# Performance work log

Measured on AMD Instinct MI355X. Metric: run time of the kernel, lower is better.

## Reference

```python
import jax, jax.numpy as jnp
import numpy as np

WIN = 7
K1, K2 = 0.01, 0.03
NP_ = WIN ** 3
COV_NORM = NP_ / (NP_ - 1)


def _box3d(x, win=WIN):
    # Separable box filter: three 1D VALID convs (same math as the dense
    for ax in range(3):
        kshape = [1, 1, 1, 1, 1]
        kshape[2 + ax] = win
        k = jnp.ones(kshape, x.dtype) / win
        x = jax.lax.conv_general_dilated(
            x, k, window_strides=(1, 1, 1), padding='VALID',
            dimension_numbers=('NCDHW', 'OIDHW', 'NCDHW'))
    return x


def setup_inputs() -> dict:
    key = jax.random.key(0)
    k1, k2 = jax.random.split(key)
    B, C, D, H, W = 4, 1, 128, 128, 128
    X = jax.random.normal(k1, (B, C, D, H, W), dtype=jnp.float32)
    Y = jax.random.normal(k2, (B, C, D, H, W), dtype=jnp.float32)
    data_range = jnp.ones((B, 1, 1, 1, 1), dtype=jnp.float32)
    return {"X": X, "Y": Y, "data_range": data_range}


def reference(X, Y, data_range):
    C1 = (K1 * data_range) ** 2
    C2 = (K2 * data_range) ** 2
    ux = _box3d(X)
    uy = _box3d(Y)
    uxx = _box3d(X * X)
    uyy = _box3d(Y * Y)
    uxy = _box3d(X * Y)
    vx = COV_NORM * (uxx - ux * ux)
    vy = COV_NORM * (uyy - uy * uy)
    vxy = COV_NORM * (uxy - ux * uy)
    A1 = 2 * ux * uy + C1
    A2 = 2 * vxy + C2
    B1 = ux ** 2 + uy ** 2 + C1
    B2 = vx + vy + C2
    S = (A1 * A2) / (B1 * B2)
    return S.mean()
```

## Files before the change

kernel.cpp:

```cpp
#include <hip/hip_runtime.h>

#define NFULL 128
#define NOUT  122

#define S1_R 34
#define S1_Q 748
#define S2_R 34
#define S2_Q 546
#define NBLK 1024

__device__ __forceinline__ void phaseA_task(const float* __restrict__ px,
                                            const float* __restrict__ py,
                                            float* __restrict__ s1p)
{
    float xs[8], ys[8];
#pragma unroll
    for (int k = 0; k < 4; ++k) {
        float2 tx = *(const float2*)(px + 2 * k);
        float2 ty = *(const float2*)(py + 2 * k);
        xs[2 * k] = tx.x; xs[2 * k + 1] = tx.y;
        ys[2 * k] = ty.x; ys[2 * k + 1] = ty.y;
    }
    float sx = 0.f, sy = 0.f, sxx = 0.f, syy = 0.f, sxy = 0.f;
#pragma unroll
    for (int k = 0; k < 7; ++k) {
        sx += xs[k]; sy += ys[k];
        sxx = fmaf(xs[k], xs[k], sxx);
        syy = fmaf(ys[k], ys[k], syy);
        sxy = fmaf(xs[k], ys[k], sxy);
    }
    float tx2 = sx - xs[0] + xs[7];
    float ty2 = sy - ys[0] + ys[7];
    float txx = sxx - xs[0] * xs[0] + xs[7] * xs[7];
    float tyy = syy - ys[0] * ys[0] + ys[7] * ys[7];
    float txy = sxy - xs[0] * ys[0] + xs[7] * ys[7];
    *(float2*)(s1p + 0 * S1_Q) = make_float2(sx,  tx2);
    *(float2*)(s1p + 1 * S1_Q) = make_float2(sy,  ty2);
    *(float2*)(s1p + 2 * S1_Q) = make_float2(sxx, txx);
    *(float2*)(s1p + 3 * S1_Q) = make_float2(syy, tyy);
    *(float2*)(s1p + 4 * S1_Q) = make_float2(sxy, txy);
}

__global__ __launch_bounds__(256, 4)
void ssim3d_kernel(const float* __restrict__ X, const float* __restrict__ Y,
                   const float* __restrict__ DR, double* __restrict__ ws, int mode)
{
    __shared__ __align__(16) float s1[5 * S1_Q];
    __shared__ __align__(16) float s2[5 * S2_Q];

    const int tid = threadIdx.x;
    int bi = blockIdx.x;
    const int bb = bi & 3;  bi >>= 2;
    const int ht = bi & 7;  bi >>= 3;
    const int wt = bi & 3;  bi >>= 2;
    const int dc = bi;

    const int h0 = ht << 4;
    const int w0 = (wt == 3) ? 90 : (wt << 5);
    const int w_hi = (wt == 3) ? 122 : ((wt == 2) ? 90 : (w0 + 32));
    const int csize = (dc < 2) ? 16 : 15;
    const int d0 = (dc < 2) ? (dc << 4) : (32 + (dc - 2) * 15);
    const int nsl = csize + 6;

    const float dr = DR[bb];
    const float c1 = (0.01f * dr) * (0.01f * dr);
    const float c2 = (0.03f * dr) * (0.03f * dr);
    const float inv_n = 1.0f / 343.0f;
    const float covn = 343.0f / 342.0f;

    const int sA  = tid & 15;
    const int rA0 = tid >> 4;
    const int rA1 = 16 + (tid >> 4);
    int grA0 = h0 + rA0; if (grA0 > NFULL - 1) grA0 = NFULL - 1;
    int grA1 = h0 + rA1; if (grA1 > NFULL - 1) grA1 = NFULL - 1;
    const int coffA = w0 + 2 * sA;

    const int sC = tid & 15, hC = tid >> 4;
    const int gh  = h0 + hC;
    const int gw0 = w0 + 2 * sC;
    const bool vh = (gh < NOUT);
    const bool vld0 = vh && (gw0 < w_hi);
    const bool vld1 = vh && (gw0 + 1 < w_hi);

    const size_t planeStride = (size_t)NFULL * NFULL;
    const size_t bbase = (size_t)bb * NFULL * planeStride;

    float2 ring[7][5];
    float2 run[5];
#pragma unroll
    for (int k = 0; k < 7; ++k)
#pragma unroll
        for (int q = 0; q < 5; ++q) ring[k][q] = make_float2(0.f, 0.f);
#pragma unroll
    for (int q = 0; q < 5; ++q) run[q] = make_float2(0.f, 0.f);
    float acc = 0.0f;

    for (int base = 0; base <= nsl; base += 7) {
#pragma unroll
        for (int u = 0; u < 7; ++u) {
            const int s = base + u;
            if (s <= nsl) {
                if (s < nsl) {
                    const int dIn = d0 + s;
                    const float* Xp = X + bbase + (size_t)dIn * planeStride;
                    const float* Yp = Y + bbase + (size_t)dIn * planeStride;
                    phaseA_task(Xp + grA0 * NFULL + coffA, Yp + grA0 * NFULL + coffA,
                                s1 + rA0 * S1_R + 2 * sA);
                    if (tid < 96)
                        phaseA_task(Xp + grA1 * NFULL + coffA, Yp + grA1 * NFULL + coffA,
                                    s1 + rA1 * S1_R + 2 * sA);
                }
                if (s >= 1) {
                    const int slot = (u + 6) % 7;
                    float2 p[5];
#pragma unroll
                    for (int q = 0; q < 5; ++q)
                        p[q] = *(const float2*)(s2 + q * S2_Q + hC * S2_R + 2 * sC);
#pragma unroll
                    for (int q = 0; q < 5; ++q) {
                        run[q].x += p[q].x - ring[slot][q].x;
                        run[q].y += p[q].y - ring[slot][q].y;
                        ring[slot][q] = p[q];
                    }
                    if (s >= 7) {
#pragma unroll
                        for (int j = 0; j < 2; ++j) {
                            const bool vld = j ? vld1 : vld0;
                            if (vld) {
                                float ux  = (j ? run[0].y : run[0].x) * inv_n;
                                float uy  = (j ? run[1].y : run[1].x) * inv_n;
                                float uxx = (j ? run[2].y : run[2].x) * inv_n;
                                float uyy = (j ? run[3].y : run[3].x) * inv_n;
                                float uxy = (j ? run[4].y : run[4].x) * inv_n;
                                float vx  = covn * (uxx - ux * ux);
                                float vy  = covn * (uyy - uy * uy);
                                float vxy = covn * (uxy - ux * uy);
                                float A1  = 2.f * ux * uy + c1;
                                float A2  = 2.f * vxy + c2;
                                float B1v = ux * ux + uy * uy + c1;
                                float B2v = vx + vy + c2;
                                acc += (A1 * A2) / (B1v * B2v);
                            }
                        }
                    }
                }
                __syncthreads();
                if (s < nsl) {
#pragma unroll
                    for (int rep = 0; rep < 2; ++rep) {
                        const int t = rep ? (256 + tid) : tid;
                        if (rep == 0 || tid < 64) {
                            const int sB  = t & 15;
                            const int tq  = t >> 4;
                            const int qB  = tq % 5;
                            const int seg = tq / 5;
                            const int r0  = seg << 2;
                            const float* src = s1 + qB * S1_Q + 2 * sB;
                            float*       dst = s2 + qB * S2_Q + 2 * sB;
                            float2 v[10];
#pragma unroll
                            for (int r = 0; r < 10; ++r)
                                v[r] = *(const float2*)(src + (r0 + r) * S1_R);
                            float ax = v[0].x, ay = v[0].y;
#pragma unroll
                            for (int r = 1; r < 7; ++r) { ax += v[r].x; ay += v[r].y; }
                            *(float2*)(dst + r0 * S2_R) = make_float2(ax, ay);
#pragma unroll
                            for (int i = 1; i < 4; ++i) {
                                ax += v[6 + i].x - v[i - 1].x;
                                ay += v[6 + i].y - v[i - 1].y;
                                *(float2*)(dst + (r0 + i) * S2_R) = make_float2(ax, ay);
                            }
                        }
                    }
                }
                __syncthreads();
            }
        }
    }

#pragma unroll
    for (int off = 32; off; off >>= 1) acc += __shfl_down(acc, off);
    if ((tid & 63) == 0) s1[tid >> 6] = acc;
    __syncthreads();
    if (tid == 0) {
        double t = (double)s1[0] + (double)s1[1] + (double)s1[2] + (double)s1[3];
        if (mode) ws[blockIdx.x] = t;
        else      atomicAdd(ws, t);
    }
}

__global__ void ssim3d_finalize(const double* __restrict__ ws, float* __restrict__ out, int mode)
{
    if (mode) {
        __shared__ double sm[4];
        const int tid = threadIdx.x;
        double t = 0.0;
        for (int i = tid; i < NBLK; i += 256) t += ws[i];
#pragma unroll
        for (int off = 32; off; off >>= 1) t += __shfl_down(t, off);
        if ((tid & 63) == 0) sm[tid >> 6] = t;
        __syncthreads();
        if (tid == 0) {
            double r = sm[0] + sm[1] + sm[2] + sm[3];
            out[0] = (float)(r * (1.0 / 7263392.0));
        }
    } else {
        if (threadIdx.x == 0)
            out[0] = (float)(ws[0] * (1.0 / 7263392.0));
    }
}

extern "C" void kernel_launch(void* const* d_in, const int* in_sizes, int n_in,
                              void* d_out, int out_size, void* d_ws, size_t ws_size,
                              hipStream_t stream)
{
    const float* X  = (const float*)d_in[0];
    const float* Y  = (const float*)d_in[1];
    const float* DR = (const float*)d_in[2];
    double* ws = (double*)d_ws;

    const int mode = (ws_size >= NBLK * sizeof(double)) ? 1 : 0;
    if (!mode) hipMemsetAsync(d_ws, 0, sizeof(double), stream);
    ssim3d_kernel<<<NBLK, 256, 0, stream>>>(X, Y, DR, ws, mode);
    ssim3d_finalize<<<1, 256, 0, stream>>>(ws, (float*)d_out, mode);
}
```

Baseline: 143.9 us.

## Double-buffer row-summed stage, fold H-direction sum into consumer, rescale SSIM math

Removes the separate H-direction sliding-sum pass and its s2 buffer. Each thread now sums 7 rows directly from a double-buffered s1 slice, which drops one __syncthreads per slice and one shared-memory round trip. The SSIM formula is rewritten on unnormalized sums with pre-scaled constants, and the divide becomes a hardware reciprocal plus one Newton step. The cost is redundant 7-row summation per thread (more LDS reads), about twice the shared memory, and slightly different rounding.

```diff
diff --git a/kernel.cpp b/kernel.cpp
--- a/kernel.cpp
+++ b/kernel.cpp
@@ -5,8 +5,7 @@
 
 #define S1_R 34
 #define S1_Q 748
-#define S2_R 34
-#define S2_Q 546
+#define S1_B 3740
 #define NBLK 1024
 
 __device__ __forceinline__ void phaseA_task(const float* __restrict__ px,
@@ -45,8 +44,7 @@
 void ssim3d_kernel(const float* __restrict__ X, const float* __restrict__ Y,
                    const float* __restrict__ DR, double* __restrict__ ws, int mode)
 {
-    __shared__ __align__(16) float s1[5 * S1_Q];
-    __shared__ __align__(16) float s2[5 * S2_Q];
+    __shared__ __align__(16) float s1[2 * S1_B];
 
     const int tid = threadIdx.x;
     int bi = blockIdx.x;
@@ -63,10 +61,11 @@
     const int nsl = csize + 6;
 
     const float dr = DR[bb];
-    const float c1 = (0.01f * dr) * (0.01f * dr);
-    const float c2 = (0.03f * dr) * (0.03f * dr);
-    const float inv_n = 1.0f / 343.0f;
-    const float covn = 343.0f / 342.0f;
+    const float c1s = (0.01f * dr) * (0.01f * dr) * 117649.0f;
+    const float c2s = (0.03f * dr) * (0.03f * dr) * 117649.0f;
+    const float tni = 1.0f / 343.0f;
+    const float kkA = 2.0f * 117649.0f / 342.0f;
+    const float kkB = 117649.0f / 342.0f;
 
     const int sA  = tid & 15;
     const int rA0 = tid >> 4;
@@ -101,75 +100,54 @@
             const int s = base + u;
             if (s <= nsl) {
                 if (s < nsl) {
+                    float* dst = s1 + (size_t)((s & 1) * S1_B);
                     const int dIn = d0 + s;
                     const float* Xp = X + bbase + (size_t)dIn * planeStride;
                     const float* Yp = Y + bbase + (size_t)dIn * planeStride;
                     phaseA_task(Xp + grA0 * NFULL + coffA, Yp + grA0 * NFULL + coffA,
-                                s1 + rA0 * S1_R + 2 * sA);
+                                dst + rA0 * S1_R + 2 * sA);
                     if (tid < 96)
                         phaseA_task(Xp + grA1 * NFULL + coffA, Yp + grA1 * NFULL + coffA,
-                                    s1 + rA1 * S1_R + 2 * sA);
+                                    dst + rA1 * S1_R + 2 * sA);
                 }
                 if (s >= 1) {
+                    const float* src = s1 + (size_t)(((s - 1) & 1) * S1_B)
+                                          + hC * S1_R + 2 * sC;
                     const int slot = (u + 6) % 7;
-                    float2 p[5];
-#pragma unroll
-                    for (int q = 0; q < 5; ++q)
-                        p[q] = *(const float2*)(s2 + q * S2_Q + hC * S2_R + 2 * sC);
 #pragma unroll
                     for (int q = 0; q < 5; ++q) {
-                        run[q].x += p[q].x - ring[slot][q].x;
-                        run[q].y += p[q].y - ring[slot][q].y;
-                        ring[slot][q] = p[q];
+                        const float* p = src + q * S1_Q;
+                        float2 h = *(const float2*)p;
+#pragma unroll
+                        for (int r = 1; r < 7; ++r) {
+                            float2 v = *(const float2*)(p + r * S1_R);
+                            h.x += v.x; h.y += v.y;
+                        }
+                        run[q].x += h.x - ring[slot][q].x;
+                        run[q].y += h.y - ring[slot][q].y;
+                        ring[slot][q] = h;
                     }
                     if (s >= 7) {
 #pragma unroll
                         for (int j = 0; j < 2; ++j) {
                             const bool vld = j ? vld1 : vld0;
                             if (vld) {
-                                float ux  = (j ? run[0].y : run[0].x) * inv_n;
-                                float uy  = (j ? run[1].y : run[1].x) * inv_n;
-                                float uxx = (j ? run[2].y : run[2].x) * inv_n;
-                                float uyy = (j ? run[3].y : run[3].x) * inv_n;
-                                float uxy = (j ? run[4].y : run[4].x) * inv_n;
-                                float vx  = covn * (uxx - ux * ux);
-                                float vy  = covn * (uyy - uy * uy);
-                                float vxy = covn * (uxy - ux * uy);
-                                float A1  = 2.f * ux * uy + c1;
-                                float A2  = 2.f * vxy + c2;
-                                float B1v = ux * ux + uy * uy + c1;
-                                float B2v = vx + vy + c2;
-                                acc += (A1 * A2) / (B1v * B2v);
-                            }
-                        }
-                    }
-                }
-                __syncthreads();
-                if (s < nsl) {
-#pragma unroll
-                    for (int rep = 0; rep < 2; ++rep) {
-                        const int t = rep ? (256 + tid) : tid;
-                        if (rep == 0 || tid < 64) {
-                            const int sB  = t & 15;
-                            const int tq  = t >> 4;
-                            const int qB  = tq % 5;
-                            const int seg = tq / 5;
-                            const int r0  = seg << 2;
-                            const float* src = s1 + qB * S1_Q + 2 * sB;
-                            float*       dst = s2 + qB * S2_Q + 2 * sB;
-                            float2 v[10];
-#pragma unroll
-                            for (int r = 0; r < 10; ++r)
-                                v[r] = *(const float2*)(src + (r0 + r) * S1_R);
-                            float ax = v[0].x, ay = v[0].y;
-#pragma unroll
-                            for (int r = 1; r < 7; ++r) { ax += v[r].x; ay += v[r].y; }
-                            *(float2*)(dst + r0 * S2_R) = make_float2(ax, ay);
-#pragma unroll
-                            for (int i = 1; i < 4; ++i) {
-                                ax += v[6 + i].x - v[i - 1].x;
-                                ay += v[6 + i].y - v[i - 1].y;
-                                *(float2*)(dst + (r0 + i) * S2_R) = make_float2(ax, ay);
+                                float Sx  = j ? run[0].y : run[0].x;
+                                float Sy  = j ? run[1].y : run[1].x;
+                                float Sxx = j ? run[2].y : run[2].x;
+                                float Syy = j ? run[3].y : run[3].x;
+                                float Sxy = j ? run[4].y : run[4].x;
+                                float P = Sx * Sy;
+                                float Q = fmaf(Sx, Sx, Sy * Sy);
+                                float A1 = fmaf(2.f, P, c1s);
+                                float A2 = fmaf(kkA, fmaf(-tni, P, Sxy), c2s);
+                                float B1 = Q + c1s;
+                                float B2 = fmaf(kkB, fmaf(-tni, Q, Sxx + Syy), c2s);
+                                float num = A1 * A2;
+                                float den = B1 * B2;
+                                float r0 = __builtin_amdgcn_rcpf(den);
+                                r0 = r0 * fmaf(-den, r0, 2.0f);
+                                acc = fmaf(num, r0, acc);
                             }
                         }
                     }
```

Result: faster. 124.0 us (-13.8%).
